# Optimization experiments

Hardware: AMD Instinct MI355X
Metric: run time of the kernel (lower is better)

## Reference

```python
import jax, jax.numpy as jnp
import numpy as np
import math


def _favor(X, W, is_query):
    # X: [B,L,H,M], W: [M,M] (shared across batch, matching tf.repeat of a single QR matrix)
    M = X.shape[-1]
    dn = 1.0 / math.sqrt(math.sqrt(M))
    X = dn * X
    diag = (jnp.sum(X * X, axis=-1) * (0.5 * dn * dn))[..., None]  # [B,L,H,1]
    dot = jnp.einsum('dm,blhm->blhd', W, X)                         # [B,L,H,M]
    if is_query:
        mx = jnp.max(X, axis=-1, keepdims=True)
    else:
        mx = jnp.max(X, axis=(1, 3), keepdims=True)  # axes (-3,-1) = (L, M)
    return (1.0 / math.sqrt(M)) * jnp.exp(dot - diag - mx + 1e-8)


def _causal_attn(qs, ks, vs):
    # qs,ks: [B,L,H,M]; vs: [B,L,H,D]. Cumulative KV-state recurrence via lax.scan.
    B, L, H, M = ks.shape
    D = vs.shape[-1]

    def step(carry, x):
        sums, snorm = carry          # [B,H,M,D], [B,H,M]
        q, k, v = x                  # [B,H,M], [B,H,M], [B,H,D]
        snorm = snorm + k
        sums = sums + k[..., :, None] * v[..., None, :]
        num = jnp.einsum('bhmd,bhm->bhd', sums, q)
        den = jnp.sum(q * snorm, axis=-1, keepdims=True)
        return (sums, snorm), num / den

    init = (jnp.zeros((B, H, M, D), qs.dtype), jnp.zeros((B, H, M), qs.dtype))
    xs = (jnp.swapaxes(qs, 0, 1), jnp.swapaxes(ks, 0, 1), jnp.swapaxes(vs, 0, 1))
    _, out = jax.lax.scan(step, init, xs)   # out: [L,B,H,D]
    return jnp.swapaxes(out, 0, 1)          # [B,L,H,D]


def _make_favor_proj(rng, M):
    # Mirrors: W ~ N(0,1); Q,_ = qr(W); Q /= norm(Q, axis=-1) (TF broadcast divides columns); Q *= sqrt(M)
    W = rng.standard_normal((M, M)).astype(np.float32)
    Q, _ = np.linalg.qr(W)
    n = np.linalg.norm(Q, axis=1)          # row norms, shape (M,)
    Q = Q / n[None, :]                     # TF broadcasting quirk: divide column j by n[j]
    return jnp.asarray(Q * math.sqrt(M), dtype=jnp.float32)


def setup_inputs() -> dict:
    B, L, d_model, H = 2, 4096, 1024, 16
    M = d_model // H
    key = jax.random.key(0)
    k1, k2, k3 = jax.random.split(key, 3)
    rng = np.random.default_rng(0)

    def dense_w(dout):
        return jnp.asarray(rng.standard_normal((d_model, dout)).astype(np.float32) * 0.02)

    return {
        'queries': jax.random.normal(k1, (B, L, d_model), jnp.float32),
        'keys': jax.random.normal(k2, (B, L, d_model), jnp.float32),
        'values': jax.random.normal(k3, (B, L, d_model), jnp.float32),
        'Wq': dense_w(H * M), 'bq': jnp.zeros((H * M,), jnp.float32),
        'Wk': dense_w(H * M), 'bk': jnp.zeros((H * M,), jnp.float32),
        'Wv': dense_w(H * M), 'bv': jnp.zeros((H * M,), jnp.float32),
        'Wo': dense_w(d_model), 'bo': jnp.zeros((d_model,), jnp.float32),
        'Wfq': _make_favor_proj(rng, M),
        'Wfk': _make_favor_proj(rng, M),
        'H': H,
    }


def reference(queries, keys, values, Wq, bq, Wk, bk, Wv, bv, Wo, bo, Wfq, Wfk, H):
    N, L, _ = queries.shape
    S = keys.shape[1]
    q = (queries @ Wq + bq).reshape(N, L, H, -1)
    k = (keys @ Wk + bk).reshape(N, S, H, -1)
    v = (values @ Wv + bv).reshape(N, S, H, -1)
    Ql = _favor(q, Wfq, is_query=True)
    Kl = _favor(k, Wfk, is_query=False)
    V = _causal_attn(Ql, Kl, v)             # [N,L,H,D]
    return V.reshape(N, L, -1) @ Wo + bo    # [N,L,d_model]
```

## Files before the change

### kernel.cpp

```cpp
#include <hip/hip_runtime.h>
#include <math.h>

#define BATCH 2
#define SEQ   4096
#define DM    1024
#define NH    16
#define MD    64
#define NROW  (BATCH*SEQ)
#define RQ    (BATCH*SEQ*NH)
#define NCHUNK 64
#define CT     64
#define DN    0.35355339059327373f
#define INV_SQRT_M 0.125f
#define PITCH 72
#define STSZ  (65*64)
#define DIAG_SCALE (0.125f * 0.0625f)

typedef unsigned short ushort_t;
typedef short bf8_t __attribute__((ext_vector_type(8)));
typedef float f4_t  __attribute__((ext_vector_type(4)));
typedef ushort_t us8_t __attribute__((ext_vector_type(8)));

__device__ static inline ushort_t f2bf(float f) {
    union { float f; unsigned u; } v; v.f = f;
    unsigned r = v.u + 0x7FFFu + ((v.u >> 16) & 1u);
    return (ushort_t)(r >> 16);
}
__device__ static inline float bf2f(ushort_t u) {
    union { unsigned u; float f; } v; v.u = ((unsigned)u) << 16;
    return v.f;
}

__device__ static inline void async_ld16(const ushort_t* g, ushort_t* l) {
    __builtin_amdgcn_global_load_lds(
        (const __attribute__((address_space(1))) unsigned int*)g,
        (__attribute__((address_space(3))) unsigned int*)l,
        16, 0, 0);
}

__device__ static inline void sbar() {
    __builtin_amdgcn_sched_barrier(0);
    __builtin_amdgcn_s_barrier();
    __builtin_amdgcn_sched_barrier(0);
}
#define VMCNT(n) do { asm volatile("s_waitcnt vmcnt(" #n ")" ::: "memory"); \
                      __builtin_amdgcn_sched_barrier(0); } while (0)

#define BUFE (256*64)

__device__ static inline void g256_compute(
    const ushort_t* As, const ushort_t* Bs, int wr, int wc,
    int quad, int l15, f4_t acc[8][4])
{
    #pragma unroll
    for (int ks = 0; ks < 2; ++ks) {
        bf8_t af[8], bfr[4];
        const int slot = ((ks << 2) | quad) ^ (l15 & 7);
        #pragma unroll
        for (int i = 0; i < 8; ++i) {
            const int row = wr * 128 + i * 16 + l15;
            af[i] = *(const bf8_t*)&As[row * 64 + slot * 8];
        }
        #pragma unroll
        for (int j = 0; j < 4; ++j) {
            const int row = wc * 64 + j * 16 + l15;
            bfr[j] = *(const bf8_t*)&Bs[row * 64 + slot * 8];
        }
        __builtin_amdgcn_s_setprio(1);
        #pragma unroll
        for (int i = 0; i < 8; ++i)
            #pragma unroll
            for (int j = 0; j < 4; ++j)
                acc[i][j] = __builtin_amdgcn_mfma_f32_16x16x32_bf16(
                    af[i], bfr[j], acc[i][j], 0, 0, 0);
        __builtin_amdgcn_s_setprio(0);
    }
}

__device__ static inline void gemm256_core(
    const ushort_t* __restrict__ A, const ushort_t* __restrict__ BT,
    ushort_t* As, ushort_t* Bs, int bm, int bn, int tid, f4_t acc[8][4])
{
    const int lane = tid & 63, w = tid >> 6;
    const int wr = w >> 2, wc = w & 3;
    const int quad = lane >> 4, l15 = lane & 15;
    const int lrow = lane >> 3;
    const int kslot = (lane & 7) ^ lrow;

    auto stage = [&](int t, int sel) {
        #pragma unroll
        for (int c = 0; c < 4; ++c) {
            const int r0 = w * 8 + c * 64;
            const int r = r0 + lrow;
            const ushort_t* ga = A  + (size_t)(bm + r) * DM + t * 64 + kslot * 8;
            const ushort_t* gb = BT + (size_t)(bn + r) * DM + t * 64 + kslot * 8;
            async_ld16(ga, &As[sel * BUFE + r0 * 64]);
            async_ld16(gb, &Bs[sel * BUFE + r0 * 64]);
        }
    };

    stage(0, 0);
    stage(1, 1);
    VMCNT(8);
    sbar();

    #pragma unroll 1
    for (int tt = 0; tt < 7; ++tt) {
        g256_compute(&As[0],    &Bs[0],    wr, wc, quad, l15, acc);
        sbar();
        stage(2 * tt + 2, 0);
        VMCNT(8);
        sbar();

        g256_compute(&As[BUFE], &Bs[BUFE], wr, wc, quad, l15, acc);
        sbar();
        stage(2 * tt + 3, 1);
        VMCNT(8);
        sbar();
    }
    g256_compute(&As[0], &Bs[0], wr, wc, quad, l15, acc);
    VMCNT(0);
    sbar();
    g256_compute(&As[BUFE], &Bs[BUFE], wr, wc, quad, l15, acc);
}

__device__ static inline void swz128(int bx, int* bm, int* bn) {
    const int nid = (bx & 7) * 16 + (bx >> 3);
    *bm = (nid >> 2) << 8;
    *bn = (nid & 3) << 8;
}

__global__ __launch_bounds__(256) void prep_weights(
    const float* __restrict__ W0, const float* __restrict__ W1,
    const float* __restrict__ W2, const float* __restrict__ W3,
    ushort_t* __restrict__ WT, unsigned* __restrict__ kmOrd)
{
    if (blockIdx.z == 0 && blockIdx.x == 0 && blockIdx.y == 0 && threadIdx.x < 32)
        kmOrd[threadIdx.x] = 0u;
    const float* W = blockIdx.z == 0 ? W0 : (blockIdx.z == 1 ? W1 : (blockIdx.z == 2 ? W2 : W3));
    ushort_t* dst = WT + (size_t)blockIdx.z * DM * DM;
    __shared__ float t[32][33];
    const int k0 = blockIdx.x * 32, n0 = blockIdx.y * 32;
    const int tx = threadIdx.x & 31, ty = threadIdx.x >> 5;
    #pragma unroll
    for (int r = 0; r < 32; r += 8)
        t[ty + r][tx] = W[(size_t)(k0 + ty + r) * 1024 + n0 + tx];
    __syncthreads();
    #pragma unroll
    for (int r = 0; r < 32; r += 8)
        dst[(size_t)(n0 + ty + r) * 1024 + k0 + tx] = f2bf(t[tx][ty + r]);
}

__global__ __launch_bounds__(256) void cvt_qkv(
    const float* __restrict__ Q, const float* __restrict__ K,
    const float* __restrict__ V, ushort_t* __restrict__ Y)
{
    const int y = blockIdx.y;
    const float* X = y == 0 ? Q : (y == 1 ? K : V);
    ushort_t* dst = Y + (size_t)y * NROW * DM;
    int i = blockIdx.x * 256 + threadIdx.x;
    const float4* X4 = (const float4*)X;
    float4 a = X4[i * 2], b = X4[i * 2 + 1];
    us8_t o;
    o[0]=f2bf(a.x); o[1]=f2bf(a.y); o[2]=f2bf(a.z); o[3]=f2bf(a.w);
    o[4]=f2bf(b.x); o[5]=f2bf(b.y); o[6]=f2bf(b.z); o[7]=f2bf(b.w);
    *(us8_t*)&dst[i * 8] = o;
}

__global__ __launch_bounds__(512, 2) void gemm_qkv(
    const ushort_t* __restrict__ Xc, const ushort_t* __restrict__ WT,
    const float* __restrict__ bq, const float* __restrict__ bk,
    const float* __restrict__ bv, ushort_t* __restrict__ Obase,
    unsigned* __restrict__ kmOrd)
{
    __shared__ ushort_t As[2 * BUFE];
    __shared__ ushort_t Bs[2 * BUFE];
    const int z = blockIdx.y;
    const ushort_t* A  = Xc + (size_t)z * NROW * DM;
    const ushort_t* BT = WT + (size_t)z * DM * DM;
    const float* bias = z == 0 ? bq : (z == 1 ? bk : bv);
    ushort_t* Cbf = Obase + (size_t)z * NROW * DM;

    const int tid = threadIdx.x;
    int bm, bn;
    swz128(blockIdx.x, &bm, &bn);
    const int lane = tid & 63, w = tid >> 6;
    const int wr = w >> 2, wc = w & 3;
    const int quad = lane >> 4, l15 = lane & 15;

    f4_t acc[8][4] = {};
    gemm256_core(A, BT, As, Bs, bm, bn, tid, acc);

    float mx = -3.4e38f;
    #pragma unroll
    for (int j = 0; j < 4; ++j) {
        const int col = bn + wc * 64 + j * 16 + l15;
        const float bb = bias[col];
        #pragma unroll
        for (int i = 0; i < 8; ++i) {
            const int row0 = bm + wr * 128 + i * 16 + quad * 4;
            #pragma unroll
            for (int r = 0; r < 4; ++r) {
                float v = acc[i][j][r] + bb;
                mx = fmaxf(mx, v);
                Cbf[(size_t)(row0 + r) * DM + col] = f2bf(v);
            }
        }
    }
    if (z == 1) {
        #pragma unroll
        for (int off = 32; off; off >>= 1) mx = fmaxf(mx, __shfl_xor(mx, off));
        if (lane == 0) {
            const int b = bm >> 12;
            const int h = (bn + wc * 64) >> 6;
            unsigned ub = __float_as_uint(mx);
            unsigned enc = (ub & 0x80000000u) ? ~ub : (ub | 0x80000000u);
            atomicMax(&kmOrd[b * NH + h], enc);
        }
    }
}

__global__ __launch_bounds__(512, 2) void gemm_out(
    const ushort_t* __restrict__ A, const ushort_t* __restrict__ BT,
    const float* __restrict__ bias, float* __restrict__ C)
{
    __shared__ ushort_t As[2 * BUFE];
    __shared__ ushort_t Bs[2 * BUFE];
    const int tid = threadIdx.x;
    int bm, bn;
    swz128(blockIdx.x, &bm, &bn);
    const int lane = tid & 63, w = tid >> 6;
    const int wr = w >> 2, wc = w & 3;
    const int quad = lane >> 4, l15 = lane & 15;

    f4_t acc[8][4] = {};
    gemm256_core(A, BT, As, Bs, bm, bn, tid, acc);

    #pragma unroll
    for (int j = 0; j < 4; ++j) {
        const int col = bn + wc * 64 + j * 16 + l15;
        const float bb = bias[col];
        #pragma unroll
        for (int i = 0; i < 8; ++i) {
            const int row0 = bm + wr * 128 + i * 16 + quad * 4;
            #pragma unroll
            for (int r = 0; r < 4; ++r)
                C[(size_t)(row0 + r) * DM + col] = acc[i][j][r] + bb;
        }
    }
}

__global__ __launch_bounds__(256) void favor_k_mfma(
    ushort_t* __restrict__ X, const float* __restrict__ Wf,
    const unsigned* __restrict__ kmOrd)
{
    __shared__ ushort_t Xs[64 * PITCH];
    __shared__ ushort_t Ws[64 * PITCH];
    __shared__ float ssp[64][4];
    __shared__ float diag[64], mxr[64];
    const int tid = threadIdx.x;
    const int lane = tid & 63, w = tid >> 6;
    const int quad = lane >> 4, l15 = lane & 15;
    const int rbase = blockIdx.x * 64;

    #pragma unroll
    for (int r = 0; r < 2; ++r) {
        int idx = tid + r * 256;
        int row = idx >> 3, ch = idx & 7;
        *(us8_t*)&Xs[row * PITCH + ch * 8] =
            *(const us8_t*)&X[(size_t)(rbase + row) * 64 + ch * 8];
    }
    const float4* Wf4 = (const float4*)Wf;
    #pragma unroll
    for (int i = 0; i < 4; ++i) {
        int f4i = tid + i * 256;
        int row = f4i >> 4, q4 = f4i & 15;
        float4 wv = Wf4[f4i];
        Ws[row * PITCH + q4 * 4 + 0] = f2bf(DN * wv.x);
        Ws[row * PITCH + q4 * 4 + 1] = f2bf(DN * wv.y);
        Ws[row * PITCH + q4 * 4 + 2] = f2bf(DN * wv.z);
        Ws[row * PITCH + q4 * 4 + 3] = f2bf(DN * wv.w);
    }
    __syncthreads();

    {
        const int row = tid >> 2, seg = tid & 3;
        const us8_t* xp = (const us8_t*)&Xs[row * PITCH + seg * 16];
        us8_t a = xp[0], b2 = xp[1];
        float ss = 0.f;
        #pragma unroll
        for (int j = 0; j < 8; ++j) {
            float x0 = bf2f(a[j]), x1 = bf2f(b2[j]);
            ss += x0 * x0 + x1 * x1;
        }
        ssp[row][seg] = ss;
    }
    __syncthreads();
    if (tid < 64) {
        diag[tid] = (ssp[tid][0] + ssp[tid][1] + ssp[tid][2] + ssp[tid][3]) * DIAG_SCALE;
        int rg = rbase + tid;
        int h = rg & (NH - 1);
        int b = rg >> 16;
        unsigned u = kmOrd[b * NH + h];
        unsigned bits = (u & 0x80000000u) ? (u & 0x7FFFFFFFu) : ~u;
        mxr[tid] = DN * __uint_as_float(bits);
    }
    __syncthreads();

    bf8_t xf[2];
    #pragma unroll
    for (int ks = 0; ks < 2; ++ks)
        xf[ks] = *(const bf8_t*)&Xs[(w * 16 + l15) * PITCH + ks * 32 + quad * 8];
    f4_t acc[4] = {};
    #pragma unroll
    for (int dt = 0; dt < 4; ++dt)
        #pragma unroll
        for (int ks = 0; ks < 2; ++ks) {
            bf8_t wfr = *(const bf8_t*)&Ws[(dt * 16 + l15) * PITCH + ks * 32 + quad * 8];
            acc[dt] = __builtin_amdgcn_mfma_f32_16x16x32_bf16(xf[ks], wfr, acc[dt], 0, 0, 0);
        }
    __syncthreads();

    #pragma unroll
    for (int r = 0; r < 4; ++r) {
        int row = w * 16 + quad * 4 + r;
        float d_ = diag[row], m_ = mxr[row];
        #pragma unroll
        for (int dt = 0; dt < 4; ++dt) {
            float e = acc[dt][r] - d_ - m_ + 1e-8f;
            X[(size_t)(rbase + row) * 64 + dt * 16 + l15] = f2bf(INV_SQRT_M * expf(e));
        }
    }
}

__global__ __launch_bounds__(256) void chunk_sums_mfma(
    const ushort_t* __restrict__ Kbf, const ushort_t* __restrict__ Vbf,
    ushort_t* __restrict__ ST)
{
    const int bx = blockIdx.x;
    const int c = bx & 63, h = (bx >> 6) & 15, b = bx >> 10;
    __shared__ ushort_t Kt[64 * PITCH];
    __shared__ ushort_t Vt[80 * PITCH];
    const int tid = threadIdx.x;
    const int lane = tid & 63, w = tid >> 6;
    const int quad = lane >> 4, l15 = lane & 15;

    const size_t gbase = ((size_t)(b * SEQ + c * CT)) * DM + h * MD;
    #pragma unroll
    for (int r = 0; r < 2; ++r) {
        int ch = w + r * 4;
        int t = lane;
        us8_t kv = *(const us8_t*)&Kbf[gbase + (size_t)t * DM + ch * 8];
        us8_t vv = *(const us8_t*)&Vbf[gbase + (size_t)t * DM + ch * 8];
        #pragma unroll
        for (int j = 0; j < 8; ++j) {
            Kt[(ch * 8 + j) * PITCH + t] = kv[j];
            Vt[(ch * 8 + j) * PITCH + t] = vv[j];
        }
    }
    if (tid < 64) Vt[64 * PITCH + tid] = (ushort_t)0x3F80;
    __syncthreads();

    ushort_t* Sg = ST + (size_t)((b * NH + h) * NCHUNK + c) * STSZ;

    bf8_t vf[2];
    #pragma unroll
    for (int ks = 0; ks < 2; ++ks)
        vf[ks] = *(const bf8_t*)&Vt[(w * 16 + l15) * PITCH + ks * 32 + quad * 8];
    f4_t acc[4] = {};
    #pragma unroll
    for (int mt = 0; mt < 4; ++mt)
        #pragma unroll
        for (int ks = 0; ks < 2; ++ks) {
            bf8_t kf = *(const bf8_t*)&Kt[(mt * 16 + l15) * PITCH + ks * 32 + quad * 8];
            acc[mt] = __builtin_amdgcn_mfma_f32_16x16x32_bf16(vf[ks], kf, acc[mt], 0, 0, 0);
        }
    #pragma unroll
    for (int mt = 0; mt < 4; ++mt)
        #pragma unroll
        for (int r = 0; r < 4; ++r)
            Sg[(w * 16 + quad * 4 + r) * 64 + mt * 16 + l15] = f2bf(acc[mt][r]);

    if (w == 0) {
        bf8_t vf4[2];
        #pragma unroll
        for (int ks = 0; ks < 2; ++ks)
            vf4[ks] = *(const bf8_t*)&Vt[(64 + l15) * PITCH + ks * 32 + quad * 8];
        f4_t accz[4] = {};
        #pragma unroll
        for (int mt = 0; mt < 4; ++mt)
            #pragma unroll
            for (int ks = 0; ks < 2; ++ks) {
                bf8_t kf = *(const bf8_t*)&Kt[(mt * 16 + l15) * PITCH + ks * 32 + quad * 8];
                accz[mt] = __builtin_amdgcn_mfma_f32_16x16x32_bf16(vf4[ks], kf, accz[mt], 0, 0, 0);
            }
        if (quad == 0) {
            #pragma unroll
            for (int mt = 0; mt < 4; ++mt)
                Sg[64 * 64 + mt * 16 + l15] = f2bf(accz[mt][0]);
        }
    }
}

__global__ __launch_bounds__(256) void prefix_scan_st(ushort_t* __restrict__ ST)
{
    const int sb = blockIdx.x / 17;
    const int e = (blockIdx.x % 17) * 256 + threadIdx.x;
    if (e >= STSZ) return;
    ushort_t* p = ST + (size_t)sb * NCHUNK * STSZ + e;
    ushort_t v[NCHUNK];
    #pragma unroll
    for (int c = 0; c < NCHUNK; ++c) v[c] = p[(size_t)c * STSZ];
    float run = 0.f;
    #pragma unroll
    for (int c = 0; c < NCHUNK; ++c) {
        float cur = bf2f(v[c]);
        p[(size_t)c * STSZ] = f2bf(run);
        run += cur;
    }
}

__global__ __launch_bounds__(256) void intra_attn_mfma(
    const ushort_t* __restrict__ Qraw, const ushort_t* __restrict__ Kbf,
    const ushort_t* __restrict__ Vbf, const ushort_t* __restrict__ ST,
    const float* __restrict__ Wfq, ushort_t* __restrict__ Obf)
{
    const int bx = blockIdx.x;
    const int c = bx & 63, h = (bx >> 6) & 15, b = bx >> 10;
    __shared__ ushort_t Qs[64 * PITCH];
    __shared__ ushort_t Ks[64 * PITCH];
    __shared__ ushort_t Vt[80 * PITCH];
    __shared__ ushort_t St[80 * PITCH];
    __shared__ ushort_t Ws[64 * PITCH];
    __shared__ float ssp[64][4];
    __shared__ float mxp[64][4];
    __shared__ float diag[64], mxr[64], dens[64];
    const int tid = threadIdx.x;
    const int lane = tid & 63, w = tid >> 6;
    const int quad = lane >> 4, l15 = lane & 15;

    const size_t gbase = ((size_t)(b * SEQ + c * CT)) * DM + h * MD;

    #pragma unroll
    for (int r = 0; r < 2; ++r) {
        int idx = tid + r * 256;
        int row = idx >> 3, ch = idx & 7;
        us8_t qv = *(const us8_t*)&Qraw[gbase + (size_t)row * DM + ch * 8];
        us8_t kv = *(const us8_t*)&Kbf[gbase + (size_t)row * DM + ch * 8];
        *(us8_t*)&Qs[row * PITCH + ch * 8] = qv;
        *(us8_t*)&Ks[row * PITCH + ch * 8] = kv;
    }
    #pragma unroll
    for (int r = 0; r < 2; ++r) {
        int ch = w + r * 4;
        int t = lane;
        us8_t vv = *(const us8_t*)&Vbf[gbase + (size_t)t * DM + ch * 8];
        #pragma unroll
        for (int j = 0; j < 8; ++j) Vt[(ch * 8 + j) * PITCH + t] = vv[j];
    }
    #pragma unroll
    for (int r = 0; r < 4; ++r) {
        int idx = tid + r * 256;
        int row = 64 + (idx >> 6), t = idx & 63;
        Vt[row * PITCH + t] = (row == 64) ? (ushort_t)0x3F80 : (ushort_t)0;
    }
    const us8_t* Sg8 = (const us8_t*)(ST + (size_t)((b * NH + h) * NCHUNK + c) * STSZ);
    #pragma unroll
    for (int r = 0; r < 3; ++r) {
        int idx = tid + r * 256;
        if (idx < 520) {
            int d = idx >> 3, mo = (idx & 7) * 8;
            *(us8_t*)&St[d * PITCH + mo] = Sg8[idx];
        }
        int idx2 = idx - 520;
        if (idx2 >= 0 && idx2 < 120) {
            int row = 65 + (idx2 >> 3), mo = (idx2 & 7) * 8;
            us8_t z = {};
            *(us8_t*)&St[row * PITCH + mo] = z;
        }
    }
    const float4* Wf4 = (const float4*)Wfq;
    #pragma unroll
    for (int i = 0; i < 4; ++i) {
        int f4i = tid + i * 256;
        int row = f4i >> 4, q4 = f4i & 15;
        float4 wv = Wf4[f4i];
        Ws[row * PITCH + q4 * 4 + 0] = f2bf(DN * wv.x);
        Ws[row * PITCH + q4 * 4 + 1] = f2bf(DN * wv.y);
        Ws[row * PITCH + q4 * 4 + 2] = f2bf(DN * wv.z);
        Ws[row * PITCH + q4 * 4 + 3] = f2bf(DN * wv.w);
    }
    __syncthreads();

    {
        const int row = tid >> 2, seg = tid & 3;
        const us8_t* xp = (const us8_t*)&Qs[row * PITCH + seg * 16];
        us8_t a = xp[0], b2 = xp[1];
        float ss = 0.f, mx = -3.4e38f;
        #pragma unroll
        for (int j = 0; j < 8; ++j) {
            float x0 = bf2f(a[j]), x1 = bf2f(b2[j]);
            ss += x0 * x0 + x1 * x1;
            mx = fmaxf(mx, fmaxf(x0, x1));
        }
        ssp[row][seg] = ss;
        mxp[row][seg] = mx;
    }
    __syncthreads();
    if (tid < 64) {
        diag[tid] = (ssp[tid][0] + ssp[tid][1] + ssp[tid][2] + ssp[tid][3]) * DIAG_SCALE;
        mxr[tid] = DN * fmaxf(fmaxf(mxp[tid][0], mxp[tid][1]),
                              fmaxf(mxp[tid][2], mxp[tid][3]));
    }
    __syncthreads();

    {
        bf8_t xf[2];
        #pragma unroll
        for (int ks = 0; ks < 2; ++ks)
            xf[ks] = *(const bf8_t*)&Qs[(w * 16 + l15) * PITCH + ks * 32 + quad * 8];
        f4_t facc[4] = {};
        #pragma unroll
        for (int dt = 0; dt < 4; ++dt)
            #pragma unroll
            for (int ks = 0; ks < 2; ++ks) {
                bf8_t wfr = *(const bf8_t*)&Ws[(dt * 16 + l15) * PITCH + ks * 32 + quad * 8];
                facc[dt] = __builtin_amdgcn_mfma_f32_16x16x32_bf16(xf[ks], wfr, facc[dt], 0, 0, 0);
            }
        __syncthreads();
        #pragma unroll
        for (int r = 0; r < 4; ++r) {
            int row = w * 16 + quad * 4 + r;
            float d_ = diag[row], m_ = mxr[row];
            #pragma unroll
            for (int dt = 0; dt < 4; ++dt) {
                float e = facc[dt][r] - d_ - m_ + 1e-8f;
                Qs[row * PITCH + dt * 16 + l15] = f2bf(INV_SQRT_M * expf(e));
            }
        }
    }
    __syncthreads();

    bf8_t qf[2];
    #pragma unroll
    for (int ks = 0; ks < 2; ++ks)
        qf[ks] = *(const bf8_t*)&Qs[(w * 16 + l15) * PITCH + ks * 32 + quad * 8];
    f4_t accA[4] = {};
    #pragma unroll
    for (int jt = 0; jt < 4; ++jt)
        #pragma unroll
        for (int ks = 0; ks < 2; ++ks) {
            bf8_t kf = *(const bf8_t*)&Ks[(jt * 16 + l15) * PITCH + ks * 32 + quad * 8];
            accA[jt] = __builtin_amdgcn_mfma_f32_16x16x32_bf16(qf[ks], kf, accA[jt], 0, 0, 0);
        }
    __syncthreads();
    #pragma unroll
    for (int jt = 0; jt < 4; ++jt) {
        int j = jt * 16 + l15;
        #pragma unroll
        for (int r = 0; r < 4; ++r) {
            int i = w * 16 + quad * 4 + r;
            float a = (j <= i) ? accA[jt][r] : 0.f;
            Ks[i * PITCH + j] = f2bf(a);
        }
    }
    __syncthreads();

    bf8_t af[2];
    #pragma unroll
    for (int ks = 0; ks < 2; ++ks)
        af[ks] = *(const bf8_t*)&Ks[(w * 16 + l15) * PITCH + ks * 32 + quad * 8];
    f4_t acc[5] = {};
    #pragma unroll
    for (int dt = 0; dt < 5; ++dt)
        #pragma unroll
        for (int ks = 0; ks < 2; ++ks) {
            bf8_t sf = *(const bf8_t*)&St[(dt * 16 + l15) * PITCH + ks * 32 + quad * 8];
            acc[dt] = __builtin_amdgcn_mfma_f32_16x16x32_bf16(qf[ks], sf, acc[dt], 0, 0, 0);
            bf8_t vf = *(const bf8_t*)&Vt[(dt * 16 + l15) * PITCH + ks * 32 + quad * 8];
            acc[dt] = __builtin_amdgcn_mfma_f32_16x16x32_bf16(af[ks], vf, acc[dt], 0, 0, 0);
        }
    if (l15 == 0) {
        #pragma unroll
        for (int r = 0; r < 4; ++r) dens[w * 16 + quad * 4 + r] = acc[4][r];
    }
    __syncthreads();

    #pragma unroll
    for (int r = 0; r < 4; ++r) {
        int i = w * 16 + quad * 4 + r;
        float inv = 1.0f / dens[i];
        #pragma unroll
        for (int dt = 0; dt < 4; ++dt)
            Obf[gbase + (size_t)i * DM + dt * 16 + l15] = f2bf(acc[dt][r] * inv);
    }
}

extern "C" void kernel_launch(void* const* d_in, const int* in_sizes, int n_in,
                              void* d_out, int out_size, void* d_ws, size_t ws_size,
                              hipStream_t stream)
{
    const float* queries = (const float*)d_in[0];
    const float* keys    = (const float*)d_in[1];
    const float* values  = (const float*)d_in[2];
    const float* Wq = (const float*)d_in[3];  const float* bq = (const float*)d_in[4];
    const float* Wk = (const float*)d_in[5];  const float* bk = (const float*)d_in[6];
    const float* Wv = (const float*)d_in[7];  const float* bv = (const float*)d_in[8];
    const float* Wo = (const float*)d_in[9];  const float* bo = (const float*)d_in[10];
    const float* Wfq = (const float*)d_in[11];
    const float* Wfk = (const float*)d_in[12];

    char* ws = (char*)d_ws;
    unsigned* kmOrd = (unsigned*)ws;
    ushort_t* STb = (ushort_t*)(ws + 256);
    ushort_t* qbf = STb + (size_t)32 * NCHUNK * STSZ;
    ushort_t* kbf = qbf + (size_t)NROW * DM;
    ushort_t* vbf = kbf + (size_t)NROW * DM;
    ushort_t* obf = vbf + (size_t)NROW * DM;
    ushort_t* xcvt = obf + (size_t)NROW * DM;
    ushort_t* wT  = xcvt + (size_t)3 * NROW * DM;
    ushort_t* WoT = wT + (size_t)3 * DM * DM;

    prep_weights<<<dim3(32, 32, 4), 256, 0, stream>>>(Wq, Wk, Wv, Wo, wT, kmOrd);

    const int n8 = NROW * DM / 8;
    cvt_qkv<<<dim3(n8 / 256, 3), 256, 0, stream>>>(queries, keys, values, xcvt);

    gemm_qkv<<<dim3(128, 3), 512, 0, stream>>>(xcvt, wT, bq, bk, bv, qbf, kmOrd);

    favor_k_mfma<<<RQ / 64, 256, 0, stream>>>(kbf, Wfk, kmOrd);

    chunk_sums_mfma<<<BATCH * NH * NCHUNK, 256, 0, stream>>>(kbf, vbf, STb);
    prefix_scan_st<<<32 * 17, 256, 0, stream>>>(STb);
    intra_attn_mfma<<<BATCH * NH * NCHUNK, 256, 0, stream>>>(qbf, kbf, vbf, STb, Wfq, obf);

    gemm_out<<<128, 512, 0, stream>>>(obf, WoT, bo, (float*)d_out);
}
```

Before: 339.9 us.

## Shrink GEMM tiles to 128x256 with finer-grained interleaved async staging

Replaces the 256x256 GEMM tile with a 128x256 tile in both the QKV and output projections, doubling the grid from 128 to 256 blocks so all CUs on the device have work. The main loop is restructured to split the A loads into two halves and interleave LDS reads, global async loads and MFMA groups at finer granularity, with a new XCD-aware block swizzle. This trades more redundant B-tile loads per output element for better CU occupancy and overlap. It also cuts the accumulator register footprint per wave.

```diff
diff --git a/kernel.cpp b/kernel.cpp
--- a/kernel.cpp
+++ b/kernel.cpp
@@ -46,88 +46,122 @@
 #define VMCNT(n) do { asm volatile("s_waitcnt vmcnt(" #n ")" ::: "memory"); \
                       __builtin_amdgcn_sched_barrier(0); } while (0)
 
-#define BUFE (256*64)
-
-__device__ static inline void g256_compute(
-    const ushort_t* As, const ushort_t* Bs, int wr, int wc,
-    int quad, int l15, f4_t acc[8][4])
-{
-    #pragma unroll
-    for (int ks = 0; ks < 2; ++ks) {
-        bf8_t af[8], bfr[4];
-        const int slot = ((ks << 2) | quad) ^ (l15 & 7);
-        #pragma unroll
-        for (int i = 0; i < 8; ++i) {
-            const int row = wr * 128 + i * 16 + l15;
-            af[i] = *(const bf8_t*)&As[row * 64 + slot * 8];
-        }
-        #pragma unroll
-        for (int j = 0; j < 4; ++j) {
-            const int row = wc * 64 + j * 16 + l15;
-            bfr[j] = *(const bf8_t*)&Bs[row * 64 + slot * 8];
-        }
-        __builtin_amdgcn_s_setprio(1);
-        #pragma unroll
-        for (int i = 0; i < 8; ++i)
-            #pragma unroll
-            for (int j = 0; j < 4; ++j)
-                acc[i][j] = __builtin_amdgcn_mfma_f32_16x16x32_bf16(
-                    af[i], bfr[j], acc[i][j], 0, 0, 0);
-        __builtin_amdgcn_s_setprio(0);
-    }
-}
-
-__device__ static inline void gemm256_core(
+__device__ static inline void gemm128_core(
     const ushort_t* __restrict__ A, const ushort_t* __restrict__ BT,
-    ushort_t* As, ushort_t* Bs, int bm, int bn, int tid, f4_t acc[8][4])
+    ushort_t* As, ushort_t* Bs, int bm, int bn, int tid, f4_t acc[4][4])
 {
     const int lane = tid & 63, w = tid >> 6;
     const int wr = w >> 2, wc = w & 3;
     const int quad = lane >> 4, l15 = lane & 15;
     const int lrow = lane >> 3;
-    const int kslot = (lane & 7) ^ lrow;
-
-    auto stage = [&](int t, int sel) {
+    const int kcol = ((lane & 7) ^ lrow) * 8;
+
+    auto stB = [&](int t, int s) {
         #pragma unroll
         for (int c = 0; c < 4; ++c) {
-            const int r0 = w * 8 + c * 64;
-            const int r = r0 + lrow;
-            const ushort_t* ga = A  + (size_t)(bm + r) * DM + t * 64 + kslot * 8;
-            const ushort_t* gb = BT + (size_t)(bn + r) * DM + t * 64 + kslot * 8;
-            async_ld16(ga, &As[sel * BUFE + r0 * 64]);
-            async_ld16(gb, &Bs[sel * BUFE + r0 * 64]);
+            const int r0 = c * 64 + w * 8;
+            async_ld16(BT + (size_t)(bn + r0 + lrow) * DM + t * 64 + kcol,
+                       &Bs[s * 16384 + r0 * 64]);
         }
     };
-
-    stage(0, 0);
-    stage(1, 1);
-    VMCNT(8);
+    auto stA1 = [&](int t, int s) {
+        const int r0 = (w < 4) ? w * 8 : 32 + w * 8;
+        async_ld16(A + (size_t)(bm + r0 + lrow) * DM + t * 64 + kcol,
+                   &As[s * 8192 + r0 * 64]);
+    };
+    auto stA2 = [&](int t, int s) {
+        const int r0 = (w < 4) ? 32 + w * 8 : 64 + w * 8;
+        async_ld16(A + (size_t)(bm + r0 + lrow) * DM + t * 64 + kcol,
+                   &As[s * 8192 + r0 * 64]);
+    };
+
+    auto loadB = [&](int s, bf8_t bf[2][4]) {
+        #pragma unroll
+        for (int ks = 0; ks < 2; ++ks) {
+            const int slot8 = (((ks << 2) | quad) ^ (l15 & 7)) * 8;
+            #pragma unroll
+            for (int j = 0; j < 4; ++j) {
+                const int row = wc * 64 + j * 16 + l15;
+                bf[ks][j] = *(const bf8_t*)&Bs[s * 16384 + row * 64 + slot8];
+            }
+        }
+    };
+    auto loadA = [&](int s, int ih, bf8_t af[2][2]) {
+        #pragma unroll
+        for (int ks = 0; ks < 2; ++ks) {
+            const int slot8 = (((ks << 2) | quad) ^ (l15 & 7)) * 8;
+            #pragma unroll
+            for (int i = 0; i < 2; ++i) {
+                const int row = wr * 64 + (ih * 2 + i) * 16 + l15;
+                af[ks][i] = *(const bf8_t*)&As[s * 8192 + row * 64 + slot8];
+            }
+        }
+    };
+    auto mfma16 = [&](int ih, bf8_t af[2][2], bf8_t bf[2][4]) {
+        __builtin_amdgcn_s_setprio(1);
+        #pragma unroll
+        for (int ks = 0; ks < 2; ++ks)
+            #pragma unroll
+            for (int i = 0; i < 2; ++i)
+                #pragma unroll
+                for (int j = 0; j < 4; ++j)
+                    acc[ih * 2 + i][j] = __builtin_amdgcn_mfma_f32_16x16x32_bf16(
+                        af[ks][i], bf[ks][j], acc[ih * 2 + i][j], 0, 0, 0);
+        __builtin_amdgcn_s_setprio(0);
+    };
+
+    stB(0, 0); stA1(0, 0);
+    stA2(0, 0);
+    stB(1, 1); stA1(1, 1);
+    VMCNT(6);
     sbar();
 
+    bf8_t bf[2][4], af[2][2];
     #pragma unroll 1
-    for (int tt = 0; tt < 7; ++tt) {
-        g256_compute(&As[0],    &Bs[0],    wr, wc, quad, l15, acc);
+    for (int v = 0; v < 7; ++v) {
+        const int u0 = 2 * v;
+        loadB(0, bf); loadA(0, 0, af);
+        stA2(u0 + 1, 1);
+        VMCNT(6); sbar();
+        mfma16(0, af, bf);
         sbar();
-        stage(2 * tt + 2, 0);
-        VMCNT(8);
+        loadA(0, 1, af);
+        stB(u0 + 2, 0); stA1(u0 + 2, 0);
+        VMCNT(6); sbar();
+        mfma16(1, af, bf);
         sbar();
-
-        g256_compute(&As[BUFE], &Bs[BUFE], wr, wc, quad, l15, acc);
+        loadB(1, bf); loadA(1, 0, af);
+        stA2(u0 + 2, 0);
+        VMCNT(6); sbar();
+        mfma16(0, af, bf);
         sbar();
-        stage(2 * tt + 3, 1);
-        VMCNT(8);
+        loadA(1, 1, af);
+        stB(u0 + 3, 1); stA1(u0 + 3, 1);
+        VMCNT(6); sbar();
+        mfma16(1, af, bf);
         sbar();
     }
-    g256_compute(&As[0], &Bs[0], wr, wc, quad, l15, acc);
-    VMCNT(0);
+    loadB(0, bf); loadA(0, 0, af);
+    stA2(15, 1);
+    VMCNT(6); sbar();
+    mfma16(0, af, bf);
     sbar();
-    g256_compute(&As[BUFE], &Bs[BUFE], wr, wc, quad, l15, acc);
-}
-
-__device__ static inline void swz128(int bx, int* bm, int* bn) {
-    const int nid = (bx & 7) * 16 + (bx >> 3);
-    *bm = (nid >> 2) << 8;
-    *bn = (nid & 3) << 8;
+    loadA(0, 1, af);
+    VMCNT(1); sbar();
+    mfma16(1, af, bf);
+    sbar();
+    loadB(1, bf); loadA(1, 0, af);
+    VMCNT(0); sbar();
+    mfma16(0, af, bf);
+    sbar();
+    loadA(1, 1, af);
+    mfma16(1, af, bf);
+}
+
+__device__ static inline void swz256(int bx, int* bm, int* bn) {
+    const int xcd = bx & 7, s = bx >> 3;
+    *bm = (xcd * 8 + (s >> 2)) << 7;
+    *bn = (s & 3) << 8;
 }
 
 __global__ __launch_bounds__(256) void prep_weights(
@@ -173,8 +207,8 @@
     const float* __restrict__ bv, ushort_t* __restrict__ Obase,
     unsigned* __restrict__ kmOrd)
 {
-    __shared__ ushort_t As[2 * BUFE];
-    __shared__ ushort_t Bs[2 * BUFE];
+    __shared__ ushort_t As[2 * 8192];
+    __shared__ ushort_t Bs[2 * 16384];
     const int z = blockIdx.y;
     const ushort_t* A  = Xc + (size_t)z * NROW * DM;
     const ushort_t* BT = WT + (size_t)z * DM * DM;
@@ -183,13 +217,13 @@
 
     const int tid = threadIdx.x;
     int bm, bn;
-    swz128(blockIdx.x, &bm, &bn);
+    swz256(blockIdx.x, &bm, &bn);
     const int lane = tid & 63, w = tid >> 6;
     const int wr = w >> 2, wc = w & 3;
     const int quad = lane >> 4, l15 = lane & 15;
 
-    f4_t acc[8][4] = {};
-    gemm256_core(A, BT, As, Bs, bm, bn, tid, acc);
+    f4_t acc[4][4] = {};
+    gemm128_core(A, BT, As, Bs, bm, bn, tid, acc);
 
     float mx = -3.4e38f;
     #pragma unroll
@@ -197,8 +231,8 @@
         const int col = bn + wc * 64 + j * 16 + l15;
         const float bb = bias[col];
         #pragma unroll
-        for (int i = 0; i < 8; ++i) {
-            const int row0 = bm + wr * 128 + i * 16 + quad * 4;
+        for (int i = 0; i < 4; ++i) {
+            const int row0 = bm + wr * 64 + i * 16 + quad * 4;
             #pragma unroll
             for (int r = 0; r < 4; ++r) {
                 float v = acc[i][j][r] + bb;
@@ -224,25 +258,25 @@
     const ushort_t* __restrict__ A, const ushort_t* __restrict__ BT,
     const float* __restrict__ bias, float* __restrict__ C)
 {
-    __shared__ ushort_t As[2 * BUFE];
-    __shared__ ushort_t Bs[2 * BUFE];
+    __shared__ ushort_t As[2 * 8192];
+    __shared__ ushort_t Bs[2 * 16384];
     const int tid = threadIdx.x;
     int bm, bn;
-    swz128(blockIdx.x, &bm, &bn);
+    swz256(blockIdx.x, &bm, &bn);
     const int lane = tid & 63, w = tid >> 6;
     const int wr = w >> 2, wc = w & 3;
     const int quad = lane >> 4, l15 = lane & 15;
 
-    f4_t acc[8][4] = {};
-    gemm256_core(A, BT, As, Bs, bm, bn, tid, acc);
+    f4_t acc[4][4] = {};
+    gemm128_core(A, BT, As, Bs, bm, bn, tid, acc);
 
     #pragma unroll
     for (int j = 0; j < 4; ++j) {
         const int col = bn + wc * 64 + j * 16 + l15;
         const float bb = bias[col];
         #pragma unroll
-        for (int i = 0; i < 8; ++i) {
-            const int row0 = bm + wr * 128 + i * 16 + quad * 4;
+        for (int i = 0; i < 4; ++i) {
+            const int row0 = bm + wr * 64 + i * 16 + quad * 4;
             #pragma unroll
             for (int r = 0; r < 4; ++r)
                 C[(size_t)(row0 + r) * DM + col] = acc[i][j][r] + bb;
@@ -626,7 +660,7 @@
     const int n8 = NROW * DM / 8;
     cvt_qkv<<<dim3(n8 / 256, 3), 256, 0, stream>>>(queries, keys, values, xcvt);
 
-    gemm_qkv<<<dim3(128, 3), 512, 0, stream>>>(xcvt, wT, bq, bk, bv, qbf, kmOrd);
+    gemm_qkv<<<dim3(256, 3), 512, 0, stream>>>(xcvt, wT, bq, bk, bv, qbf, kmOrd);
 
     favor_k_mfma<<<RQ / 64, 256, 0, stream>>>(kbf, Wfk, kmOrd);
 
@@ -634,5 +668,5 @@
     prefix_scan_st<<<32 * 17, 256, 0, stream>>>(STb);
     intra_attn_mfma<<<BATCH * NH * NCHUNK, 256, 0, stream>>>(qbf, kbf, vbf, STb, Wfq, obf);
 
-    gemm_out<<<128, 512, 0, stream>>>(obf, WoT, bo, (float*)d_out);
-}
+    gemm_out<<<256, 512, 0, stream>>>(obf, WoT, bo, (float*)d_out);
+}
```

Result: faster. 319.3 us (-6.1%).

## Interleave half-tile LDS reads, MFMA and async loads in GEMM main loop

Applied to the files above, without the earlier changes.

The 256x256 GEMM core now splits each k-step into half-tiles. It issues the next stage's async global-to-LDS loads in small pieces between the LDS fragment reads and the MFMA bursts, instead of loading a whole stage after each compute phase. This spreads memory traffic more evenly across the loop to overlap it with matrix work. The QKV GEMM also moves to a flat 1-D grid with an XCD-aware block mapping so blocks sharing A rows land on the same XCD, and gemm_out gets a similar mapping. The cost is many more barriers per k-tile, and the tighter buffer reuse needs careful vmcnt accounting.

```diff
diff --git a/kernel.cpp b/kernel.cpp
--- a/kernel.cpp
+++ b/kernel.cpp
@@ -48,35 +48,6 @@
 
 #define BUFE (256*64)
 
-__device__ static inline void g256_compute(
-    const ushort_t* As, const ushort_t* Bs, int wr, int wc,
-    int quad, int l15, f4_t acc[8][4])
-{
-    #pragma unroll
-    for (int ks = 0; ks < 2; ++ks) {
-        bf8_t af[8], bfr[4];
-        const int slot = ((ks << 2) | quad) ^ (l15 & 7);
-        #pragma unroll
-        for (int i = 0; i < 8; ++i) {
-            const int row = wr * 128 + i * 16 + l15;
-            af[i] = *(const bf8_t*)&As[row * 64 + slot * 8];
-        }
-        #pragma unroll
-        for (int j = 0; j < 4; ++j) {
-            const int row = wc * 64 + j * 16 + l15;
-            bfr[j] = *(const bf8_t*)&Bs[row * 64 + slot * 8];
-        }
-        __builtin_amdgcn_s_setprio(1);
-        #pragma unroll
-        for (int i = 0; i < 8; ++i)
-            #pragma unroll
-            for (int j = 0; j < 4; ++j)
-                acc[i][j] = __builtin_amdgcn_mfma_f32_16x16x32_bf16(
-                    af[i], bfr[j], acc[i][j], 0, 0, 0);
-        __builtin_amdgcn_s_setprio(0);
-    }
-}
-
 __device__ static inline void gemm256_core(
     const ushort_t* __restrict__ A, const ushort_t* __restrict__ BT,
     ushort_t* As, ushort_t* Bs, int bm, int bn, int tid, f4_t acc[8][4])
@@ -85,49 +56,74 @@
     const int wr = w >> 2, wc = w & 3;
     const int quad = lane >> 4, l15 = lane & 15;
     const int lrow = lane >> 3;
-    const int kslot = (lane & 7) ^ lrow;
-
-    auto stage = [&](int t, int sel) {
-        #pragma unroll
-        for (int c = 0; c < 4; ++c) {
-            const int r0 = w * 8 + c * 64;
-            const int r = r0 + lrow;
-            const ushort_t* ga = A  + (size_t)(bm + r) * DM + t * 64 + kslot * 8;
-            const ushort_t* gb = BT + (size_t)(bn + r) * DM + t * 64 + kslot * 8;
-            async_ld16(ga, &As[sel * BUFE + r0 * 64]);
-            async_ld16(gb, &Bs[sel * BUFE + r0 * 64]);
+    const int kcol = ((lane & 7) ^ lrow) * 8;
+
+    auto stA = [&](int t, int s, int h) {
+        #pragma unroll
+        for (int c = 0; c < 2; ++c) {
+            const int r0 = h * 128 + c * 64 + w * 8;
+            async_ld16(A + (size_t)(bm + r0 + lrow) * DM + t * 64 + kcol,
+                       &As[s * BUFE + r0 * 64]);
         }
     };
-
-    stage(0, 0);
-    stage(1, 1);
-    VMCNT(8);
-    sbar();
+    auto stB = [&](int t, int s, int h) {
+        #pragma unroll
+        for (int c = 0; c < 2; ++c) {
+            const int r0 = h * 128 + c * 64 + w * 8;
+            async_ld16(BT + (size_t)(bn + r0 + lrow) * DM + t * 64 + kcol,
+                       &Bs[s * BUFE + r0 * 64]);
+        }
+    };
+
+    bf8_t af[4], bf[4];
+    auto rdB = [&](int s, int ks) {
+        const int slot8 = (((ks << 2) | quad) ^ (l15 & 7)) * 8;
+        #pragma unroll
+        for (int j = 0; j < 4; ++j)
+            bf[j] = *(const bf8_t*)&Bs[s * BUFE + (wc * 64 + j * 16 + l15) * 64 + slot8];
+    };
+    auto rdA = [&](int s, int ks, int ih) {
+        const int slot8 = (((ks << 2) | quad) ^ (l15 & 7)) * 8;
+        #pragma unroll
+        for (int i = 0; i < 4; ++i)
+            af[i] = *(const bf8_t*)&As[s * BUFE + (wr * 128 + (ih * 4 + i) * 16 + l15) * 64 + slot8];
+    };
+    auto mm = [&](int ih) {
+        __builtin_amdgcn_s_setprio(1);
+        #pragma unroll
+        for (int i = 0; i < 4; ++i)
+            #pragma unroll
+            for (int j = 0; j < 4; ++j)
+                acc[ih * 4 + i][j] = __builtin_amdgcn_mfma_f32_16x16x32_bf16(
+                    af[i], bf[j], acc[ih * 4 + i][j], 0, 0, 0);
+        __builtin_amdgcn_s_setprio(0);
+    };
+
+    stB(0, 0, 0); stB(0, 0, 1); stA(0, 0, 0); stA(0, 0, 1); stB(1, 1, 0);
+    VMCNT(4); sbar();
 
     #pragma unroll 1
-    for (int tt = 0; tt < 7; ++tt) {
-        g256_compute(&As[0],    &Bs[0],    wr, wc, quad, l15, acc);
-        sbar();
-        stage(2 * tt + 2, 0);
-        VMCNT(8);
-        sbar();
-
-        g256_compute(&As[BUFE], &Bs[BUFE], wr, wc, quad, l15, acc);
-        sbar();
-        stage(2 * tt + 3, 1);
-        VMCNT(8);
-        sbar();
-    }
-    g256_compute(&As[0], &Bs[0], wr, wc, quad, l15, acc);
-    VMCNT(0);
-    sbar();
-    g256_compute(&As[BUFE], &Bs[BUFE], wr, wc, quad, l15, acc);
-}
-
-__device__ static inline void swz128(int bx, int* bm, int* bn) {
-    const int nid = (bx & 7) * 16 + (bx >> 3);
-    *bm = (nid >> 2) << 8;
-    *bn = (nid & 3) << 8;
+    for (int v = 0; v < 7; ++v) {
+        const int u = 2 * v;
+        rdA(0,0,0); rdB(0,0); stB(u+1, 1, 1); VMCNT(4); sbar(); mm(0); sbar();
+        rdA(0,0,1);           stA(u+1, 1, 0); VMCNT(4); sbar(); mm(1); sbar();
+        rdA(0,1,0); rdB(0,1); stA(u+1, 1, 1); VMCNT(4); sbar(); mm(0); sbar();
+        rdA(0,1,1);           stB(u+2, 0, 0); VMCNT(4); sbar(); mm(1); sbar();
+
+        rdA(1,0,0); rdB(1,0); stB(u+2, 0, 1); VMCNT(4); sbar(); mm(0); sbar();
+        rdA(1,0,1);           stA(u+2, 0, 0); VMCNT(4); sbar(); mm(1); sbar();
+        rdA(1,1,0); rdB(1,1); stA(u+2, 0, 1); VMCNT(4); sbar(); mm(0); sbar();
+        rdA(1,1,1);           stB(u+3, 1, 0); VMCNT(4); sbar(); mm(1); sbar();
+    }
+    rdA(0,0,0); rdB(0,0); stB(15, 1, 1); VMCNT(4); sbar(); mm(0); sbar();
+    rdA(0,0,1);           stA(15, 1, 0); VMCNT(4); sbar(); mm(1); sbar();
+    rdA(0,1,0); rdB(0,1); stA(15, 1, 1); VMCNT(4); sbar(); mm(0); sbar();
+    rdA(0,1,1);                           VMCNT(2); sbar(); mm(1); sbar();
+    VMCNT(0); sbar();
+    rdA(1,0,0); rdB(1,0); mm(0);
+    rdA(1,0,1);           mm(1);
+    rdA(1,1,0); rdB(1,1); mm(0);
+    rdA(1,1,1);           mm(1);
 }
 
 __global__ __launch_bounds__(256) void prep_weights(
@@ -175,15 +171,19 @@
 {
     __shared__ ushort_t As[2 * BUFE];
     __shared__ ushort_t Bs[2 * BUFE];
-    const int z = blockIdx.y;
+    const int bx = blockIdx.x;
+    const int xcd = bx & 7, idx = bx >> 3;
+    const int z = idx >> 4;
+    const int rem = idx & 15;
+    const int bm = ((xcd << 2) + (rem >> 2)) << 8;
+    const int bn = (rem & 3) << 8;
+
     const ushort_t* A  = Xc + (size_t)z * NROW * DM;
     const ushort_t* BT = WT + (size_t)z * DM * DM;
     const float* bias = z == 0 ? bq : (z == 1 ? bk : bv);
     ushort_t* Cbf = Obase + (size_t)z * NROW * DM;
 
     const int tid = threadIdx.x;
-    int bm, bn;
-    swz128(blockIdx.x, &bm, &bn);
     const int lane = tid & 63, w = tid >> 6;
     const int wr = w >> 2, wc = w & 3;
     const int quad = lane >> 4, l15 = lane & 15;
@@ -226,9 +226,12 @@
 {
     __shared__ ushort_t As[2 * BUFE];
     __shared__ ushort_t Bs[2 * BUFE];
+    const int bx = blockIdx.x;
+    const int xcd = bx & 7, idx = bx >> 3;
+    const int bm = ((xcd << 2) + (idx >> 2)) << 8;
+    const int bn = (idx & 3) << 8;
+
     const int tid = threadIdx.x;
-    int bm, bn;
-    swz128(blockIdx.x, &bm, &bn);
     const int lane = tid & 63, w = tid >> 6;
     const int wr = w >> 2, wc = w & 3;
     const int quad = lane >> 4, l15 = lane & 15;
@@ -626,7 +629,7 @@
     const int n8 = NROW * DM / 8;
     cvt_qkv<<<dim3(n8 / 256, 3), 256, 0, stream>>>(queries, keys, values, xcvt);
 
-    gemm_qkv<<<dim3(128, 3), 512, 0, stream>>>(xcvt, wT, bq, bk, bv, qbf, kmOrd);
+    gemm_qkv<<<384, 512, 0, stream>>>(xcvt, wT, bq, bk, bv, qbf, kmOrd);
 
     favor_k_mfma<<<RQ / 64, 256, 0, stream>>>(kbf, Wfk, kmOrd);
 
```

Result: no change. 342.6 us (+0.8%).
